# Optimization experiments

Measured on AMD Instinct MI355X. Metric: run time of the kernel, lower is better.

Reference implementation:

```python
import jax, jax.numpy as jnp
import numpy as np

N = 1_048_576   # nodes
E = 8_388_608   # edges
G = 32_768      # graphs
D = 9           # node embedding dim (hardcoded emb_dim=9 in source)
H = 2 * D       # GIN MLP hidden
L = 3           # num_layers
ATOM_V, BOND_V = 119, 6
BN_EPS = 1e-5


def setup_inputs() -> dict:
    key = jax.random.key(0)
    ks = jax.random.split(key, 12)
    f = lambda i, shape: jax.random.normal(ks[i], shape, jnp.float32) * 0.1
    return {
        'atom_emb': f(0, (9, ATOM_V, D)),
        'bond_emb': f(1, (L, 3, BOND_V, D)),
        'eps_gin': jnp.zeros((L,), jnp.float32),
        'W1': f(2, (L, D, H)), 'b1': jnp.zeros((L, H)),
        'bn1_g': jnp.ones((L, H)), 'bn1_b': jnp.zeros((L, H)),
        'W2': f(3, (L, H, D)), 'b2': jnp.zeros((L, D)),
        'bno_g': jnp.ones((L, D)), 'bno_b': jnp.zeros((L, D)),
        'vnW1': f(4, (L - 1, D, H)), 'vnb1': jnp.zeros((L - 1, H)),
        'vnbn1_g': jnp.ones((L - 1, H)), 'vnbn1_b': jnp.zeros((L - 1, H)),
        'vnW2': f(5, (L - 1, H, D)), 'vnb2': jnp.zeros((L - 1, D)),
        'vnbn2_g': jnp.ones((L - 1, D)), 'vnbn2_b': jnp.zeros((L - 1, D)),
        'x': jax.random.randint(ks[6], (N, 9), 0, 2),
        'edge_index': jax.random.randint(ks[7], (2, E), 0, N),
        'edge_attr': jax.random.randint(ks[8], (E, 3), 0, 2),
        'batch': jnp.sort(jax.random.randint(ks[9], (N,), 0, G)),
        'num_graphs': G,
    }


def _bn(h, g, b):
    # BatchNorm1d in training mode: batch mean / biased variance
    m = h.mean(axis=0)
    v = h.var(axis=0)
    return (h - m) * jax.lax.rsqrt(v + BN_EPS) * g + b


def reference(atom_emb, bond_emb, eps_gin, W1, b1, bn1_g, bn1_b, W2, b2,
              bno_g, bno_b, vnW1, vnb1, vnbn1_g, vnbn1_b, vnW2, vnb2,
              vnbn2_g, vnbn2_b, x, edge_index, edge_attr, batch, num_graphs):
    n_nodes = x.shape[0]
    src, dst = edge_index[0], edge_index[1]
    # AtomEncoder: sum of per-field embeddings -> [N, D]
    h = atom_emb[jnp.arange(atom_emb.shape[0])[None, :], x].sum(axis=1)
    vn = jnp.zeros((num_graphs, h.shape[1]), h.dtype)  # virtualnode emb init 0
    num_layers = W1.shape[0]
    for l in range(num_layers):
        h_in = h + vn[batch]                              # broadcast VN to nodes
        # BondEncoder for this layer -> [E, D]
        e = bond_emb[l][jnp.arange(3)[None, :], edge_attr].sum(axis=1)
        # GIN message: relu(x_j + e), sum-aggregate at target
        msg = jax.nn.relu(h_in[src] + e)
        aggr = jax.ops.segment_sum(msg, dst, num_segments=n_nodes)
        z = (1.0 + eps_gin[l]) * h_in + aggr
        z = jax.nn.relu(_bn(z @ W1[l] + b1[l], bn1_g[l], bn1_b[l])) @ W2[l] + b2[l]
        z = _bn(z, bno_g[l], bno_b[l])
        if l < num_layers - 1:
            z = jax.nn.relu(z)
        h_new = z + h_in                                   # residual=True
        if l < num_layers - 1:
            vn_tmp = jax.ops.segment_sum(h_in, batch, num_segments=num_graphs) + vn
            t = jax.nn.relu(_bn(vn_tmp @ vnW1[l] + vnb1[l], vnbn1_g[l], vnbn1_b[l]))
            t = jax.nn.relu(_bn(t @ vnW2[l] + vnb2[l], vnbn2_g[l], vnbn2_b[l]))
            vn = vn + t                                    # VN residual
        h = h_new
    pooled = jax.ops.segment_sum(h, batch, num_segments=num_graphs)  # global_add_pool
    return jnp.sum(pooled, axis=0, keepdims=True)          # [1, D]
```

## Files before the change

kernel.cpp:

```cpp
#include <hip/hip_runtime.h>
#include <hip/hip_fp8.h>

#define NN 1048576
#define NE 8388608
#define NG 32768
#define DD 9
#define SB 12
#define HH 18
#define BN_EPS 1e-5f

#define NPB 512
#define NB  2048
#define NGRP 64
#define P1B 512
#define P3MAX 5120

#define NSUM1 0
#define NSQ1  18
#define NSUM2 36
#define NSQ2  45
#define OUTS  54
#define VBASE 4096
#define VSUM1 (VBASE+0)
#define VSQ1  (VBASE+18)
#define VSUM2 (VBASE+36)
#define VSQ2  (VBASE+45)
#define STATS_FLOATS 4224

typedef float fv4 __attribute__((ext_vector_type(4)));

__device__ __forceinline__ float waveReduce(float v) {
#pragma unroll
  for (int off = 32; off > 0; off >>= 1) v += __shfl_down(v, off, 64);
  return v;
}
__device__ __forceinline__ unsigned f8enc(float f) {
  __hip_fp8_e4m3 v(f);
  return (unsigned)v.__x;
}
__device__ __forceinline__ float f8dec(unsigned b) {
  __hip_fp8_e4m3 v;
  v.__x = (__hip_fp8_storage_t)b;
  return (float)v;
}


__global__ void __launch_bounds__(1024)
k_counthist(const int* __restrict__ ei, int* __restrict__ cnt_pad,
            int* __restrict__ blkcnt) {
  __shared__ int hist[NB];
  int tid = threadIdx.x;
  for (int i = tid; i < NB; i += 1024) hist[i] = 0;
  __syncthreads();
  const int CH = NE / P1B;
  int base = blockIdx.x * CH;
  for (int i = tid; i < CH; i += 1024)
    atomicAdd(&hist[ei[NE + base + i] >> 9], 1);
  __syncthreads();
  for (int i = tid; i < NB; i += 1024)
    if (hist[i]) atomicAdd(&cnt_pad[i * 16], hist[i]);
  if (tid < NGRP) {
    int s = 0;
#pragma unroll
    for (int k = 0; k < 32; ++k) s += hist[tid * 32 + k];
    blkcnt[tid * P1B + blockIdx.x] = s;
  }
}

__global__ void k_scan(const int* __restrict__ cnt_pad, int* __restrict__ bucket_base,
                       int* __restrict__ bucket_cursor) {
  __shared__ int tsum[256];
  int tid = threadIdx.x;
  int c[8];
  int run = 0;
#pragma unroll
  for (int k = 0; k < 8; ++k) { c[k] = cnt_pad[(tid * 8 + k) * 16]; run += c[k]; }
  tsum[tid] = run;
  __syncthreads();
  for (int off = 1; off < 256; off <<= 1) {
    int v = (tid >= off) ? tsum[tid - off] : 0;
    __syncthreads();
    tsum[tid] += v;
    __syncthreads();
  }
  int excl = tsum[tid] - run;
#pragma unroll
  for (int k = 0; k < 8; ++k) {
    bucket_base[tid * 8 + k] = excl;
    bucket_cursor[tid * 8 + k] = excl;
    excl += c[k];
  }
  if (tid == 255) bucket_base[NB] = tsum[255];
}

__global__ void k_scanG(int* __restrict__ blkcnt, const int* __restrict__ bucket_base) {
  __shared__ int tsum[256];
  int tid = threadIdx.x;
  int g = blockIdx.x;
  int c0 = blkcnt[g * P1B + 2 * tid], c1 = blkcnt[g * P1B + 2 * tid + 1];
  int run = c0 + c1;
  tsum[tid] = run;
  __syncthreads();
  for (int off = 1; off < 256; off <<= 1) {
    int v = (tid >= off) ? tsum[tid - off] : 0;
    __syncthreads();
    tsum[tid] += v;
    __syncthreads();
  }
  int excl = tsum[tid] - run + bucket_base[g << 5];
  blkcnt[g * P1B + 2 * tid] = excl;
  blkcnt[g * P1B + 2 * tid + 1] = excl + c0;
}

__global__ void __launch_bounds__(1024)
k_p1(const int* __restrict__ ei, const int* __restrict__ ea,
     const int* __restrict__ blkcnt, uint2* __restrict__ coarse) {
  __shared__ int lcnt[NGRP];
  __shared__ int lbase[NGRP];
  int tid = threadIdx.x;
  if (tid < NGRP) { lcnt[tid] = 0; lbase[tid] = blkcnt[tid * P1B + blockIdx.x]; }
  __syncthreads();
  const int CH = NE / P1B;
  int base = blockIdx.x * CH;
  for (int k = 0; k < CH / 1024; ++k) {
    int e = base + k * 1024 + tid;
    int s = ei[e];
    int d = ei[NE + e];
    unsigned at = (unsigned)((ea[(size_t)e * 3 + 0] & 1) |
                             ((ea[(size_t)e * 3 + 1] & 1) << 1) |
                             ((ea[(size_t)e * 3 + 2] & 1) << 2));
    int g = d >> 14;
    int pos = atomicAdd(&lcnt[g], 1);
    coarse[lbase[g] + pos] = make_uint2((unsigned)s | (at << 20), (unsigned)d);
  }
}

#define P2K 48
#define P2SUB 32
__global__ void __launch_bounds__(256)
k_p2(const uint2* __restrict__ coarse, const int* __restrict__ bucket_base,
     int* __restrict__ bucket_cursor, unsigned* __restrict__ binned) {
  __shared__ unsigned stage[32 * P2K];
  __shared__ int scnt[32], gbase[32];
  int tid = threadIdx.x;
  int g = blockIdx.x >> 5;
  int sub = blockIdx.x & 31;
  int s0 = bucket_base[g << 5];
  int s1 = bucket_base[(g + 1) << 5];
  int len = s1 - s0;
  int chunk = (len + P2SUB - 1) >> 5;
  int my0 = s0 + sub * chunk;
  int my1 = min(my0 + chunk, s1);
  if (tid < 32) scnt[tid] = 0;
  __syncthreads();
  for (int b0 = my0; b0 < my1; b0 += 1024) {
#pragma unroll
    for (int k = 0; k < 4; ++k) {
      int i = b0 + k * 256 + tid;
      if (i < my1) {
        uint2 rec = coarse[i];
        unsigned s = rec.x & 0xFFFFFu;
        unsigned at = rec.x >> 20;
        unsigned d = rec.y;
        int bt = (int)((d >> 9) & 31u);
        unsigned o = s | ((d & 511u) << 20) | (at << 29);
        int pos = atomicAdd(&scnt[bt], 1);
        if (pos < P2K) stage[bt * P2K + pos] = o;
        else binned[atomicAdd(&bucket_cursor[(g << 5) | bt], 1)] = o;
      }
    }
    __syncthreads();
    {
      int bt = tid >> 3, j = tid & 7;
      int cnt = min(scnt[bt], P2K);
      if (j == 0) gbase[bt] = cnt ? atomicAdd(&bucket_cursor[(g << 5) | bt], cnt) : 0;
      __syncthreads();
      for (int i = j; i < cnt; i += 8) binned[gbase[bt] + i] = stage[bt * P2K + i];
    }
    __syncthreads();
    if (tid < 32) scnt[tid] = 0;
    __syncthreads();
  }
}

__global__ void __launch_bounds__(256)
k_p3(unsigned* __restrict__ binned, const int* __restrict__ bucket_base,
     int* __restrict__ row_ptr) {
  __shared__ int cnt[512];
  __shared__ int tsum[256];
  __shared__ unsigned stage[P3MAX];
  int tid = threadIdx.x;
  int b = blockIdx.x;
  int s0 = bucket_base[b], s1 = bucket_base[b + 1];
  int len = s1 - s0;
  for (int i = tid; i < 512; i += 256) cnt[i] = 0;
  __syncthreads();
  for (int i = tid; i < len; i += 256) {
    unsigned rec = binned[s0 + i];
    atomicAdd(&cnt[(rec >> 20) & 511u], 1);
  }
  __syncthreads();
  int c0 = cnt[2 * tid], c1 = cnt[2 * tid + 1];
  int run = c0 + c1;
  tsum[tid] = run;
  __syncthreads();
  for (int off = 1; off < 256; off <<= 1) {
    int v = (tid >= off) ? tsum[tid - off] : 0;
    __syncthreads();
    tsum[tid] += v;
    __syncthreads();
  }
  int excl = tsum[tid] - run;
  row_ptr[b * NPB + 2 * tid] = s0 + excl;
  row_ptr[b * NPB + 2 * tid + 1] = s0 + excl + c0;
  if (b == NB - 1 && tid == 255) row_ptr[NN] = s0 + excl + c0 + c1;
  __syncthreads();
  cnt[2 * tid] = excl;
  cnt[2 * tid + 1] = excl + c0;
  __syncthreads();
  for (int i = tid; i < len; i += 256) {
    unsigned rec = binned[s0 + i];
    int pos = atomicAdd(&cnt[(rec >> 20) & 511u], 1);
    stage[pos] = (rec & 0xFFFFFu) | ((rec >> 29) << 20);
  }
  __syncthreads();
  for (int i = tid; i < len; i += 256) binned[s0 + i] = stage[i];
}


__device__ __forceinline__ void writeMirror(uint2* __restrict__ hmA,
                                            unsigned char* __restrict__ hmB,
                                            size_t n, const float* hv) {
  uint2 q;
  q.x = f8enc(hv[0]) | (f8enc(hv[1]) << 8) | (f8enc(hv[2]) << 16) | (f8enc(hv[3]) << 24);
  q.y = f8enc(hv[4]) | (f8enc(hv[5]) << 8) | (f8enc(hv[6]) << 16) | (f8enc(hv[7]) << 24);
  hmA[n] = q;
  hmB[n] = (unsigned char)f8enc(hv[8]);
}

__global__ void k_atom(const float* __restrict__ atom_emb, const int* __restrict__ x,
                       const int* __restrict__ batch, float* __restrict__ h,
                       uint2* __restrict__ hmA, unsigned char* __restrict__ hmB,
                       float* __restrict__ vnsum) {
  int n = blockIdx.x * 256 + threadIdx.x;
  int xi[9];
#pragma unroll
  for (int f = 0; f < 9; ++f) xi[f] = x[(size_t)n * 9 + f];
  float acc[DD] = {0.f,0.f,0.f,0.f,0.f,0.f,0.f,0.f,0.f};
#pragma unroll
  for (int f = 0; f < 9; ++f) {
    const float* row = atom_emb + ((size_t)f * 119 + xi[f]) * DD;
#pragma unroll
    for (int d = 0; d < DD; ++d) acc[d] += row[d];
  }
  float* o = h + (size_t)n * SB;
  ((float4*)o)[0] = make_float4(acc[0], acc[1], acc[2], acc[3]);
  ((float4*)o)[1] = make_float4(acc[4], acc[5], acc[6], acc[7]);
  o[8] = acc[8];
  writeMirror(hmA, hmB, (size_t)n, acc);
  int g = batch[n];
  int lane = threadIdx.x & 63;
  float s[DD];
#pragma unroll
  for (int d = 0; d < DD; ++d) s[d] = acc[d];
#pragma unroll
  for (int st = 1; st < 64; st <<= 1) {
    int gu = __shfl_up(g, st, 64);
    bool ok = (lane >= st) && (gu == g);
#pragma unroll
    for (int d = 0; d < DD; ++d) {
      float vu = __shfl_up(s[d], st, 64);
      if (ok) s[d] += vu;
    }
  }
  int gn = __shfl_down(g, 1, 64);
  if ((lane == 63) || (gn != g)) {
#pragma unroll
    for (int d = 0; d < DD; ++d) atomicAdd(&vnsum[(size_t)g * DD + d], s[d]);
  }
}

__device__ __forceinline__ void edgeDecodeAcc(unsigned r, uint2 q, unsigned db,
                                              const float* __restrict__ comb,
                                              float* __restrict__ acc) {
  const float* cb = comb + (r >> 20) * DD;
  float hv[DD] = {f8dec(q.x & 255u), f8dec((q.x >> 8) & 255u),
                  f8dec((q.x >> 16) & 255u), f8dec(q.x >> 24),
                  f8dec(q.y & 255u), f8dec((q.y >> 8) & 255u),
                  f8dec((q.y >> 16) & 255u), f8dec(q.y >> 24),
                  f8dec(db)};
#pragma unroll
  for (int d = 0; d < DD; ++d) {
    float m = hv[d] + cb[d];
    m = m > 0.f ? m : 0.f;
    acc[d] += m;
  }
}

__device__ __forceinline__ void accumNode(const unsigned* __restrict__ binned,
                                          int e0, int e1,
                                          const uint2* __restrict__ hmA,
                                          const unsigned char* __restrict__ hmB,
                                          const float* __restrict__ comb,
                                          float* __restrict__ acc) {
  int i = e0;
  for (; i + 4 <= e1; i += 4) {
    unsigned r0 = binned[i], r1 = binned[i + 1], r2 = binned[i + 2], r3 = binned[i + 3];
    uint2 q0 = hmA[r0 & 0xFFFFFu];
    uint2 q1 = hmA[r1 & 0xFFFFFu];
    uint2 q2 = hmA[r2 & 0xFFFFFu];
    uint2 q3 = hmA[r3 & 0xFFFFFu];
    unsigned char d0 = hmB[r0 & 0xFFFFFu];
    unsigned char d1 = hmB[r1 & 0xFFFFFu];
    unsigned char d2 = hmB[r2 & 0xFFFFFu];
    unsigned char d3 = hmB[r3 & 0xFFFFFu];
    edgeDecodeAcc(r0, q0, d0, comb, acc);
    edgeDecodeAcc(r1, q1, d1, comb, acc);
    edgeDecodeAcc(r2, q2, d2, comb, acc);
    edgeDecodeAcc(r3, q3, d3, comb, acc);
  }
  for (; i < e1; ++i) {
    unsigned r = binned[i];
    uint2 q = hmA[r & 0xFFFFFu];
    unsigned char db = hmB[r & 0xFFFFFu];
    edgeDecodeAcc(r, q, db, comb, acc);
  }
}

__global__ void __launch_bounds__(256, 8)
k_edgeA(const float* __restrict__ hbuf, const uint2* __restrict__ hmA,
        const unsigned char* __restrict__ hmB, const unsigned* __restrict__ binned,
        const int* __restrict__ row_ptr, const float* __restrict__ bond,
        const float* __restrict__ W1l, const float* __restrict__ b1l,
        const float* __restrict__ epsp, float* __restrict__ X,
        float* __restrict__ stats) {
  __shared__ float comb[8 * DD];
  __shared__ float sW1[DD * HH], sb1[HH], ssum[HH], ssq[HH];
  int tid = threadIdx.x;
  for (int i = tid; i < DD * HH; i += 256) sW1[i] = W1l[i];
  if (tid < 8 * DD) {
    int c = tid / DD, d = tid % DD;
    comb[tid] = bond[(0 * 6 + (c & 1)) * DD + d] +
                bond[(1 * 6 + ((c >> 1) & 1)) * DD + d] +
                bond[(2 * 6 + ((c >> 2) & 1)) * DD + d];
  }
  if (tid < HH) { sb1[tid] = b1l[tid]; ssum[tid] = 0.f; ssq[tid] = 0.f; }
  __syncthreads();

  int b = blockIdx.x;
  int nA = b * NPB + tid;
  int nB = nA + 256;
  int ea0 = row_ptr[nA], ea1 = row_ptr[nA + 1];
  int eb0 = row_ptr[nB], eb1 = row_ptr[nB + 1];
  float acc0[DD] = {0.f,0.f,0.f,0.f,0.f,0.f,0.f,0.f,0.f};
  float acc1[DD] = {0.f,0.f,0.f,0.f,0.f,0.f,0.f,0.f,0.f};
  accumNode(binned, ea0, ea1, hmA, hmB, comb, acc0);
  accumNode(binned, eb0, eb1, hmA, hmB, comb, acc1);

  float eps1 = 1.0f + epsp[0];
  float z0[DD], z1[DD];
  {
    const float* hr = hbuf + (size_t)nA * SB;
    float4 HA = ((const float4*)hr)[0], HB = ((const float4*)hr)[1];
    float h8 = hr[8];
    float hi[DD] = {HA.x, HA.y, HA.z, HA.w, HB.x, HB.y, HB.z, HB.w, h8};
#pragma unroll
    for (int d = 0; d < DD; ++d) z0[d] = eps1 * hi[d] + acc0[d];
    float* xo = X + (size_t)nA * SB;
    fv4 v0 = {z0[0], z0[1], z0[2], z0[3]};
    fv4 v1 = {z0[4], z0[5], z0[6], z0[7]};
    __builtin_nontemporal_store(v0, (fv4*)xo);
    __builtin_nontemporal_store(v1, (fv4*)(xo + 4));
    __builtin_nontemporal_store(z0[8], xo + 8);
  }
  {
    const float* hr = hbuf + (size_t)nB * SB;
    float4 HA = ((const float4*)hr)[0], HB = ((const float4*)hr)[1];
    float h8 = hr[8];
    float hi[DD] = {HA.x, HA.y, HA.z, HA.w, HB.x, HB.y, HB.z, HB.w, h8};
#pragma unroll
    for (int d = 0; d < DD; ++d) z1[d] = eps1 * hi[d] + acc1[d];
    float* xo = X + (size_t)nB * SB;
    fv4 v0 = {z1[0], z1[1], z1[2], z1[3]};
    fv4 v1 = {z1[4], z1[5], z1[6], z1[7]};
    __builtin_nontemporal_store(v0, (fv4*)xo);
    __builtin_nontemporal_store(v1, (fv4*)(xo + 4));
    __builtin_nontemporal_store(z1[8], xo + 8);
  }
  int lane0 = ((tid & 63) == 0);
#pragma unroll
  for (int j = 0; j < HH; ++j) {
    float a0 = sb1[j], a1 = sb1[j];
#pragma unroll
    for (int d = 0; d < DD; ++d) {
      a0 += z0[d] * sW1[d * HH + j];
      a1 += z1[d] * sW1[d * HH + j];
    }
    float rs = waveReduce(a0 + a1);
    float rq = waveReduce(a0 * a0 + a1 * a1);
    if (lane0) { atomicAdd(&ssum[j], rs); atomicAdd(&ssq[j], rq); }
  }
  __syncthreads();
  int copy = (b & 63) * 64;
  if (tid < HH) {
    atomicAdd(&stats[copy + NSUM1 + tid], ssum[tid]);
    atomicAdd(&stats[copy + NSQ1 + tid], ssq[tid]);
  }
}

__global__ void __launch_bounds__(256)
k_partB(float* __restrict__ X, const float* __restrict__ W1l, const float* __restrict__ b1l,
        const float* __restrict__ g1, const float* __restrict__ be1,
        const float* __restrict__ W2l, const float* __restrict__ b2l,
        float* __restrict__ stats) {
  __shared__ float sW1[DD * HH], sW2[HH * DD], sb1[HH], sb2[DD];
  __shared__ float sc1[HH], sh1[HH], ssum[DD], ssq[DD];
  int tid = threadIdx.x;
  for (int i = tid; i < DD * HH; i += 256) sW1[i] = W1l[i];
  for (int i = tid; i < HH * DD; i += 256) sW2[i] = W2l[i];
  if (tid < HH) {
    float s = 0.f, q = 0.f;
#pragma unroll
    for (int c = 0; c < 64; ++c) {
      s += stats[c * 64 + NSUM1 + tid];
      q += stats[c * 64 + NSQ1 + tid];
    }
    float mean = s * (1.0f / NN);
    float var = q * (1.0f / NN) - mean * mean;
    float sc = g1[tid] * rsqrtf(var + BN_EPS);
    sc1[tid] = sc;
    sh1[tid] = be1[tid] - mean * sc;
    sb1[tid] = b1l[tid];
  }
  if (tid < DD) { sb2[tid] = b2l[tid]; ssum[tid] = 0.f; ssq[tid] = 0.f; }
  __syncthreads();
  size_t n = (size_t)blockIdx.x * 256 + tid;
  float* xr = X + n * SB;
  fv4 XA = __builtin_nontemporal_load((const fv4*)xr);
  fv4 XB = __builtin_nontemporal_load((const fv4*)(xr + 4));
  float x8 = __builtin_nontemporal_load(xr + 8);
  float z[DD] = {XA.x, XA.y, XA.z, XA.w, XB.x, XB.y, XB.z, XB.w, x8};
  float t[HH];
#pragma unroll
  for (int j = 0; j < HH; ++j) {
    float a = sb1[j];
#pragma unroll
    for (int d = 0; d < DD; ++d) a += z[d] * sW1[d * HH + j];
    a = a * sc1[j] + sh1[j];
    t[j] = a > 0.f ? a : 0.f;
  }
  float z2[DD];
  int lane0 = ((tid & 63) == 0);
#pragma unroll
  for (int d = 0; d < DD; ++d) {
    float a = sb2[d];
#pragma unroll
    for (int j = 0; j < HH; ++j) a += t[j] * sW2[j * DD + d];
    z2[d] = a;
    float rs = waveReduce(a);
    float rq = waveReduce(a * a);
    if (lane0) { atomicAdd(&ssum[d], rs); atomicAdd(&ssq[d], rq); }
  }
  fv4 v0 = {z2[0], z2[1], z2[2], z2[3]};
  fv4 v1 = {z2[4], z2[5], z2[6], z2[7]};
  __builtin_nontemporal_store(v0, (fv4*)xr);
  __builtin_nontemporal_store(v1, (fv4*)(xr + 4));
  __builtin_nontemporal_store(z2[8], xr + 8);
  __syncthreads();
  int copy = ((int)blockIdx.x & 63) * 64;
  if (tid < DD) {
    atomicAdd(&stats[copy + NSUM2 + tid], ssum[tid]);
    atomicAdd(&stats[copy + NSQ2 + tid], ssq[tid]);
  }
}

__global__ void __launch_bounds__(256)
k_partC(const float* __restrict__ X, float* __restrict__ hbuf,
        uint2* __restrict__ hmA, unsigned char* __restrict__ hmB,
        float* __restrict__ stats, const float* __restrict__ g2,
        const float* __restrict__ be2, const int* __restrict__ batch,
        const float* __restrict__ vn_next, float* __restrict__ vnsum_out,
        int do_relu) {
  __shared__ float sc[DD], sh[DD], ssum[DD];
  int tid = threadIdx.x;
  if (tid < DD) {
    float s = 0.f, q = 0.f;
#pragma unroll
    for (int c = 0; c < 64; ++c) {
      s += stats[c * 64 + NSUM2 + tid];
      q += stats[c * 64 + NSQ2 + tid];
    }
    float mean = s * (1.0f / NN);
    float var = q * (1.0f / NN) - mean * mean;
    float sg = g2[tid] * rsqrtf(var + BN_EPS);
    sc[tid] = sg;
    sh[tid] = be2[tid] - mean * sg;
    ssum[tid] = 0.f;
  }
  __syncthreads();
  size_t n = (size_t)blockIdx.x * 256 + tid;
  const float* xr = X + n * SB;
  fv4 XA = __builtin_nontemporal_load((const fv4*)xr);
  fv4 XB = __builtin_nontemporal_load((const fv4*)(xr + 4));
  float x8 = __builtin_nontemporal_load(xr + 8);
  float zv[DD] = {XA.x, XA.y, XA.z, XA.w, XB.x, XB.y, XB.z, XB.w, x8};
  float* hr = hbuf + n * SB;
  float4 HA = ((float4*)hr)[0], HB = ((float4*)hr)[1];
  float h8 = hr[8];
  float hi[DD] = {HA.x, HA.y, HA.z, HA.w, HB.x, HB.y, HB.z, HB.w, h8};
  float hv[DD];
#pragma unroll
  for (int d = 0; d < DD; ++d) {
    float z = zv[d] * sc[d] + sh[d];
    if (do_relu) z = z > 0.f ? z : 0.f;
    hv[d] = z + hi[d];
  }
  if (vn_next != nullptr) {
    int g = batch[n];
#pragma unroll
    for (int d = 0; d < DD; ++d) hv[d] += vn_next[(size_t)g * DD + d];
    ((float4*)hr)[0] = make_float4(hv[0], hv[1], hv[2], hv[3]);
    ((float4*)hr)[1] = make_float4(hv[4], hv[5], hv[6], hv[7]);
    hr[8] = hv[8];
    writeMirror(hmA, hmB, n, hv);
    if (vnsum_out != nullptr) {
      int lane = tid & 63;
      float s[DD];
#pragma unroll
      for (int d = 0; d < DD; ++d) s[d] = hv[d];
#pragma unroll
      for (int st = 1; st < 64; st <<= 1) {
        int gu = __shfl_up(g, st, 64);
        bool ok = (lane >= st) && (gu == g);
#pragma unroll
        for (int d = 0; d < DD; ++d) {
          float vu = __shfl_up(s[d], st, 64);
          if (ok) s[d] += vu;
        }
      }
      int gn = __shfl_down(g, 1, 64);
      if ((lane == 63) || (gn != g)) {
#pragma unroll
        for (int d = 0; d < DD; ++d) atomicAdd(&vnsum_out[(size_t)g * DD + d], s[d]);
      }
    }
  } else {
    int lane0 = ((tid & 63) == 0);
#pragma unroll
    for (int d = 0; d < DD; ++d) {
      float r = waveReduce(hv[d]);
      if (lane0) atomicAdd(&ssum[d], r);
    }
    __syncthreads();
    int copy = ((int)blockIdx.x & 63) * 64;
    if (tid < DD) atomicAdd(&stats[copy + OUTS + tid], ssum[tid]);
  }
}

__global__ void k_out(const float* __restrict__ stats, float* __restrict__ out) {
  int tid = threadIdx.x;
  if (tid < DD) {
    float s = 0.f;
#pragma unroll
    for (int c = 0; c < 64; ++c) s += stats[c * 64 + OUTS + tid];
    out[tid] = s;
  }
}


__global__ void k_vnA(const float* __restrict__ vnsum, const float* __restrict__ vn,
                      float* __restrict__ vt1, const float* __restrict__ W1l,
                      const float* __restrict__ b1l, float* __restrict__ stats) {
  __shared__ float sW[DD * HH], sb[HH], ssum[HH], ssq[HH];
  int tid = threadIdx.x;
  for (int i = tid; i < DD * HH; i += 256) sW[i] = W1l[i];
  if (tid < HH) { sb[tid] = b1l[tid]; ssum[tid] = 0.f; ssq[tid] = 0.f; }
  __syncthreads();
  size_t g = (size_t)blockIdx.x * 256 + tid;
  float r[DD];
#pragma unroll
  for (int d = 0; d < DD; ++d) r[d] = vnsum[g * DD + d] + vn[g * DD + d];
  int lane0 = ((tid & 63) == 0);
#pragma unroll
  for (int j = 0; j < HH; ++j) {
    float a = sb[j];
#pragma unroll
    for (int d = 0; d < DD; ++d) a += r[d] * sW[d * HH + j];
    vt1[g * HH + j] = a;
    float rs = waveReduce(a);
    float rq = waveReduce(a * a);
    if (lane0) { atomicAdd(&ssum[j], rs); atomicAdd(&ssq[j], rq); }
  }
  __syncthreads();
  if (tid < HH) {
    atomicAdd(&stats[VSUM1 + tid], ssum[tid]);
    atomicAdd(&stats[VSQ1 + tid], ssq[tid]);
  }
}

__global__ void k_vnB(const float* __restrict__ vt1, float* __restrict__ vt2,
                      const float* __restrict__ W2l, const float* __restrict__ b2l,
                      const float* __restrict__ g1, const float* __restrict__ be1,
                      float* __restrict__ stats) {
  __shared__ float sW2[HH * DD], sb2[DD], sc1[HH], sh1[HH], ssum[DD], ssq[DD];
  int tid = threadIdx.x;
  for (int i = tid; i < HH * DD; i += 256) sW2[i] = W2l[i];
  if (tid < HH) {
    float mean = stats[VSUM1 + tid] * (1.0f / NG);
    float var = stats[VSQ1 + tid] * (1.0f / NG) - mean * mean;
    float sc = g1[tid] * rsqrtf(var + BN_EPS);
    sc1[tid] = sc;
    sh1[tid] = be1[tid] - mean * sc;
  }
  if (tid < DD) { sb2[tid] = b2l[tid]; ssum[tid] = 0.f; ssq[tid] = 0.f; }
  __syncthreads();
  size_t g = (size_t)blockIdx.x * 256 + tid;
  float t[HH];
#pragma unroll
  for (int j = 0; j < HH; ++j) {
    float a = vt1[g * HH + j] * sc1[j] + sh1[j];
    t[j] = a > 0.f ? a : 0.f;
  }
  int lane0 = ((tid & 63) == 0);
#pragma unroll
  for (int d = 0; d < DD; ++d) {
    float a = sb2[d];
#pragma unroll
    for (int j = 0; j < HH; ++j) a += t[j] * sW2[j * DD + d];
    vt2[g * DD + d] = a;
    float rs = waveReduce(a);
    float rq = waveReduce(a * a);
    if (lane0) { atomicAdd(&ssum[d], rs); atomicAdd(&ssq[d], rq); }
  }
  __syncthreads();
  if (tid < DD) {
    atomicAdd(&stats[VSUM2 + tid], ssum[tid]);
    atomicAdd(&stats[VSQ2 + tid], ssq[tid]);
  }
}

__global__ void k_vnC(const float* __restrict__ vt2, float* __restrict__ vn,
                      const float* __restrict__ g2, const float* __restrict__ be2,
                      const float* __restrict__ stats) {
  __shared__ float sc[DD], sh[DD];
  int tid = threadIdx.x;
  if (tid < DD) {
    float mean = stats[VSUM2 + tid] * (1.0f / NG);
    float var = stats[VSQ2 + tid] * (1.0f / NG) - mean * mean;
    float s = g2[tid] * rsqrtf(var + BN_EPS);
    sc[tid] = s;
    sh[tid] = be2[tid] - mean * s;
  }
  __syncthreads();
  size_t g = (size_t)blockIdx.x * 256 + tid;
#pragma unroll
  for (int d = 0; d < DD; ++d) {
    float v = vt2[g * DD + d] * sc[d] + sh[d];
    v = v > 0.f ? v : 0.f;
    vn[g * DD + d] += v;
  }
}

extern "C" void kernel_launch(void* const* d_in, const int* in_sizes, int n_in,
                              void* d_out, int out_size, void* d_ws, size_t ws_size,
                              hipStream_t stream) {
  const float* atom_emb = (const float*)d_in[0];
  const float* bond_emb = (const float*)d_in[1];
  const float* eps_gin  = (const float*)d_in[2];
  const float* W1   = (const float*)d_in[3];
  const float* b1   = (const float*)d_in[4];
  const float* bn1_g = (const float*)d_in[5];
  const float* bn1_b = (const float*)d_in[6];
  const float* W2   = (const float*)d_in[7];
  const float* b2   = (const float*)d_in[8];
  const float* bno_g = (const float*)d_in[9];
  const float* bno_b = (const float*)d_in[10];
  const float* vnW1 = (const float*)d_in[11];
  const float* vnb1 = (const float*)d_in[12];
  const float* vnbn1_g = (const float*)d_in[13];
  const float* vnbn1_b = (const float*)d_in[14];
  const float* vnW2 = (const float*)d_in[15];
  const float* vnb2 = (const float*)d_in[16];
  const float* vnbn2_g = (const float*)d_in[17];
  const float* vnbn2_b = (const float*)d_in[18];
  const int* x          = (const int*)d_in[19];
  const int* edge_index = (const int*)d_in[20];
  const int* edge_attr  = (const int*)d_in[21];
  const int* batch      = (const int*)d_in[22];
  float* out = (float*)d_out;

  float* hbuf  = (float*)d_ws;
  float* X     = hbuf + (size_t)NN * SB;
  uint2* hmA   = (uint2*)(X + (size_t)NN * SB);
  unsigned char* hmB = (unsigned char*)(hmA + (size_t)NN);
  unsigned* binned = (unsigned*)(hmB + (size_t)NN);
  float* vn    = (float*)(binned + (size_t)NE);
  float* vnsum = vn + (size_t)NG * DD;
  float* vt2   = vnsum;
  float* vt1   = vnsum + (size_t)NG * DD;
  float* stats = vt1 + (size_t)NG * HH;
  int* bucket_base   = (int*)(stats + STATS_FLOATS);
  int* bucket_cursor = bucket_base + NB + 1;
  int* row_ptr       = bucket_cursor + NB;
  uint2* coarse = (uint2*)d_ws;
  int* cnt_pad  = (int*)((char*)d_ws + (size_t)NE * sizeof(uint2));
  int* blkcnt   = cnt_pad + (size_t)NB * 16;

  (void)hipMemsetAsync(cnt_pad, 0, (size_t)NB * 16 * sizeof(int), stream);
  k_counthist<<<P1B, 1024, 0, stream>>>(edge_index, cnt_pad, blkcnt);
  k_scan<<<1, 256, 0, stream>>>(cnt_pad, bucket_base, bucket_cursor);
  k_scanG<<<NGRP, 256, 0, stream>>>(blkcnt, bucket_base);
  k_p1<<<P1B, 1024, 0, stream>>>(edge_index, edge_attr, blkcnt, coarse);
  k_p2<<<NGRP * P2SUB, 256, 0, stream>>>(coarse, bucket_base, bucket_cursor, binned);
  k_p3<<<NB, 256, 0, stream>>>(binned, bucket_base, row_ptr);

  (void)hipMemsetAsync(vn, 0, (size_t)2 * NG * DD * sizeof(float), stream);
  k_atom<<<NN / 256, 256, 0, stream>>>(atom_emb, x, batch, hbuf, hmA, hmB, vnsum);

  for (int l = 0; l < 3; ++l) {
    int has_vn = (l < 2);
    (void)hipMemsetAsync(stats, 0, STATS_FLOATS * sizeof(float), stream);
    if (has_vn) {
      k_vnA<<<NG / 256, 256, 0, stream>>>(vnsum, vn, vt1, vnW1 + (size_t)l * DD * HH,
                                          vnb1 + (size_t)l * HH, stats);
      k_vnB<<<NG / 256, 256, 0, stream>>>(vt1, vt2, vnW2 + (size_t)l * HH * DD,
                                          vnb2 + (size_t)l * DD,
                                          vnbn1_g + (size_t)l * HH, vnbn1_b + (size_t)l * HH,
                                          stats);
      k_vnC<<<NG / 256, 256, 0, stream>>>(vt2, vn, vnbn2_g + (size_t)l * DD,
                                          vnbn2_b + (size_t)l * DD, stats);
    }
    k_edgeA<<<NB, 256, 0, stream>>>(hbuf, hmA, hmB, binned, row_ptr,
                                    bond_emb + (size_t)l * 3 * 6 * DD,
                                    W1 + (size_t)l * DD * HH, b1 + (size_t)l * HH,
                                    eps_gin + l, X, stats);
    k_partB<<<NN / 256, 256, 0, stream>>>(X, W1 + (size_t)l * DD * HH,
                                          b1 + (size_t)l * HH,
                                          bn1_g + (size_t)l * HH, bn1_b + (size_t)l * HH,
                                          W2 + (size_t)l * HH * DD, b2 + (size_t)l * DD,
                                          stats);
    if (l == 0)
      (void)hipMemsetAsync(vnsum, 0, (size_t)NG * DD * sizeof(float), stream);
    k_partC<<<NN / 256, 256, 0, stream>>>(X, hbuf, hmA, hmB, stats,
                                          bno_g + (size_t)l * DD, bno_b + (size_t)l * DD,
                                          batch,
                                          has_vn ? vn : nullptr,
                                          (l == 0) ? vnsum : nullptr,
                                          has_vn ? 1 : 0);
  }
  k_out<<<1, 64, 0, stream>>>(stats, out);
}
```

Before: 1.343 ms.

## Sort edges by source octant and sweep source ranges in lockstep for locality

```diff
diff --git a/kernel.cpp b/kernel.cpp
--- a/kernel.cpp
+++ b/kernel.cpp
@@ -14,6 +14,7 @@
 #define NGRP 64
 #define P1B 512
 #define P3MAX 5120
+#define P3KEYS 4096
 
 #define NSUM1 0
 #define NSQ1  18
@@ -186,22 +187,25 @@
 __global__ void __launch_bounds__(256)
 k_p3(unsigned* __restrict__ binned, const int* __restrict__ bucket_base,
      int* __restrict__ row_ptr) {
-  __shared__ int cnt[512];
+  __shared__ int cnt[P3KEYS];
   __shared__ int tsum[256];
   __shared__ unsigned stage[P3MAX];
   int tid = threadIdx.x;
   int b = blockIdx.x;
   int s0 = bucket_base[b], s1 = bucket_base[b + 1];
   int len = s1 - s0;
-  for (int i = tid; i < 512; i += 256) cnt[i] = 0;
+  for (int i = tid; i < P3KEYS; i += 256) cnt[i] = 0;
   __syncthreads();
   for (int i = tid; i < len; i += 256) {
     unsigned rec = binned[s0 + i];
-    atomicAdd(&cnt[(rec >> 20) & 511u], 1);
-  }
-  __syncthreads();
-  int c0 = cnt[2 * tid], c1 = cnt[2 * tid + 1];
-  int run = c0 + c1;
+    int key = (int)((((rec >> 20) & 511u) << 3) | ((rec & 0xFFFFFu) >> 17));
+    atomicAdd(&cnt[key], 1);
+  }
+  __syncthreads();
+  int c[16];
+  int run = 0;
+#pragma unroll
+  for (int k = 0; k < 16; ++k) { c[k] = cnt[tid * 16 + k]; run += c[k]; }
   tsum[tid] = run;
   __syncthreads();
   for (int off = 1; off < 256; off <<= 1) {
@@ -211,16 +215,20 @@
     __syncthreads();
   }
   int excl = tsum[tid] - run;
+  int sum8 = 0;
+#pragma unroll
+  for (int k = 0; k < 8; ++k) sum8 += c[k];
   row_ptr[b * NPB + 2 * tid] = s0 + excl;
-  row_ptr[b * NPB + 2 * tid + 1] = s0 + excl + c0;
-  if (b == NB - 1 && tid == 255) row_ptr[NN] = s0 + excl + c0 + c1;
-  __syncthreads();
-  cnt[2 * tid] = excl;
-  cnt[2 * tid + 1] = excl + c0;
+  row_ptr[b * NPB + 2 * tid + 1] = s0 + excl + sum8;
+  if (b == NB - 1 && tid == 255) row_ptr[NN] = s0 + excl + run;
+  int e = excl;
+#pragma unroll
+  for (int k = 0; k < 16; ++k) { cnt[tid * 16 + k] = e; e += c[k]; }
   __syncthreads();
   for (int i = tid; i < len; i += 256) {
     unsigned rec = binned[s0 + i];
-    int pos = atomicAdd(&cnt[(rec >> 20) & 511u], 1);
+    int key = (int)((((rec >> 20) & 511u) << 3) | ((rec & 0xFFFFFu) >> 17));
+    int pos = atomicAdd(&cnt[key], 1);
     stage[pos] = (rec & 0xFFFFFu) | ((rec >> 29) << 20);
   }
   __syncthreads();
@@ -297,36 +305,6 @@
   }
 }
 
-__device__ __forceinline__ void accumNode(const unsigned* __restrict__ binned,
-                                          int e0, int e1,
-                                          const uint2* __restrict__ hmA,
-                                          const unsigned char* __restrict__ hmB,
-                                          const float* __restrict__ comb,
-                                          float* __restrict__ acc) {
-  int i = e0;
-  for (; i + 4 <= e1; i += 4) {
-    unsigned r0 = binned[i], r1 = binned[i + 1], r2 = binned[i + 2], r3 = binned[i + 3];
-    uint2 q0 = hmA[r0 & 0xFFFFFu];
-    uint2 q1 = hmA[r1 & 0xFFFFFu];
-    uint2 q2 = hmA[r2 & 0xFFFFFu];
-    uint2 q3 = hmA[r3 & 0xFFFFFu];
-    unsigned char d0 = hmB[r0 & 0xFFFFFu];
-    unsigned char d1 = hmB[r1 & 0xFFFFFu];
-    unsigned char d2 = hmB[r2 & 0xFFFFFu];
-    unsigned char d3 = hmB[r3 & 0xFFFFFu];
-    edgeDecodeAcc(r0, q0, d0, comb, acc);
-    edgeDecodeAcc(r1, q1, d1, comb, acc);
-    edgeDecodeAcc(r2, q2, d2, comb, acc);
-    edgeDecodeAcc(r3, q3, d3, comb, acc);
-  }
-  for (; i < e1; ++i) {
-    unsigned r = binned[i];
-    uint2 q = hmA[r & 0xFFFFFu];
-    unsigned char db = hmB[r & 0xFFFFFu];
-    edgeDecodeAcc(r, q, db, comb, acc);
-  }
-}
-
 __global__ void __launch_bounds__(256, 8)
 k_edgeA(const float* __restrict__ hbuf, const uint2* __restrict__ hmA,
         const unsigned char* __restrict__ hmB, const unsigned* __restrict__ binned,
@@ -350,12 +328,36 @@
   int b = blockIdx.x;
   int nA = b * NPB + tid;
   int nB = nA + 256;
-  int ea0 = row_ptr[nA], ea1 = row_ptr[nA + 1];
-  int eb0 = row_ptr[nB], eb1 = row_ptr[nB + 1];
+  int iA = row_ptr[nA];
+  const int ea1 = row_ptr[nA + 1];
+  int iB = row_ptr[nB];
+  const int eb1 = row_ptr[nB + 1];
   float acc0[DD] = {0.f,0.f,0.f,0.f,0.f,0.f,0.f,0.f,0.f};
   float acc1[DD] = {0.f,0.f,0.f,0.f,0.f,0.f,0.f,0.f,0.f};
-  accumNode(binned, ea0, ea1, hmA, hmB, comb, acc0);
-  accumNode(binned, eb0, eb1, hmA, hmB, comb, acc1);
+
+#pragma unroll 1
+  for (int q = 0; q < 8; ++q) {
+    unsigned lim = (unsigned)(q + 1) << 17;
+    while (iA < ea1) {
+      unsigned r = binned[iA];
+      unsigned src = r & 0xFFFFFu;
+      if (src >= lim) break;
+      uint2 qv = hmA[src];
+      unsigned db = hmB[src];
+      edgeDecodeAcc(r, qv, db, comb, acc0);
+      ++iA;
+    }
+    while (iB < eb1) {
+      unsigned r = binned[iB];
+      unsigned src = r & 0xFFFFFu;
+      if (src >= lim) break;
+      uint2 qv = hmA[src];
+      unsigned db = hmB[src];
+      edgeDecodeAcc(r, qv, db, comb, acc1);
+      ++iB;
+    }
+    __syncthreads();
+  }
 
   float eps1 = 1.0f + epsp[0];
   float z0[DD], z1[DD];
```

Result: faster. 1.314 ms (-2.2%).
